# Optimization experiments

Hardware: AMD Instinct MI355X
Metric: run time of the kernel (lower is better)

## Reference

```python
import jax, jax.numpy as jnp
import numpy as np

L, B, D, H = 256, 128, 256, 256


def setup_inputs() -> dict:
    key = jax.random.key(0)
    ks = jax.random.split(key, 24)
    rng = np.random.default_rng(0)
    # random dependency trees: node 0 is root, head[i] < i  => reversed index
    # order (L-1 .. 0) is a valid children-before-parent topological order
    heads = np.zeros((B, L), dtype=np.int64)
    for i in range(1, L):
        heads[:, i] = rng.integers(0, i, size=B)
    parents = np.full((L, B), L, dtype=np.int32)  # parents[node, b]; root -> L (dummy slot)
    parents[1:, :] = heads[:, 1:].T
    indexes = np.tile(np.arange(L - 1, -1, -1, dtype=np.int32)[:, None], (1, B))
    inp = {
        "inputs": jax.random.normal(ks[0], (L, B, D), jnp.float32),
        "indexes": jnp.asarray(indexes),
        "parents": jnp.asarray(parents),
    }
    i = 1
    for pre in ("dt", "td"):
        for nm, out_d, in_d in (("ioux", 3 * H, D), ("iouh", 3 * H, H), ("fx", H, D), ("fh", H, H)):
            s = 1.0 / np.sqrt(in_d)
            inp[f"{pre}_{nm}_w"] = jax.random.uniform(ks[i], (out_d, in_d), jnp.float32, -s, s)
            inp[f"{pre}_{nm}_b"] = jnp.zeros((out_d,), jnp.float32)
            i += 1
    return inp


def _cell(x, sum_c, sum_h, ioux_w, ioux_b, iouh_w, iouh_b, fx_w, fx_b, fh_w, fh_b):
    # tree-LSTM node gating; dropout is identity (eval mode)
    iou = x @ ioux_w.T + ioux_b + sum_h @ iouh_w.T + iouh_b
    i, o, u = jnp.split(iou, 3, axis=1)
    i, o, u = jax.nn.sigmoid(i), jax.nn.sigmoid(o), jnp.tanh(u)
    f = jax.nn.sigmoid(x @ fx_w.T + fx_b + sum_h @ fh_w.T + fh_b)
    c = i * u + f * sum_c
    h = o * jnp.tanh(c)
    return c, h


def _dt(inputs, indexes, parents, params):
    # bottom-up: gather accumulated child sums at node, scatter-add (c,h) to parent
    L_, B_ = indexes.shape
    H_ = params[2].shape[1]
    step_x = jnp.take_along_axis(inputs, indexes[:, :, None], axis=0)  # [L,B,D]
    step_par = jnp.take_along_axis(parents, indexes, axis=0)  # [L,B]
    barange = jnp.arange(B_)

    def step(carry, xs):
        state_c, state_h, acc_c, acc_h = carry
        x, idx, par = xs
        sc = acc_c[barange, idx]  # [B,H] sum of children cells
        sh = acc_h[barange, idx]
        c, h = _cell(x, sc, sh, *params)
        state_c = state_c.at[barange, idx].set(c)
        state_h = state_h.at[barange, idx].set(h)
        acc_c = acc_c.at[barange, par].add(c)  # root's parent -> dummy slot L
        acc_h = acc_h.at[barange, par].add(h)
        return (state_c, state_h, acc_c, acc_h), None

    init = (jnp.zeros((B_, L_, H_), inputs.dtype), jnp.zeros((B_, L_, H_), inputs.dtype),
            jnp.zeros((B_, L_ + 1, H_), inputs.dtype), jnp.zeros((B_, L_ + 1, H_), inputs.dtype))
    (sc, sh, _, _), _ = jax.lax.scan(step, init, (step_x, indexes, step_par))
    return sc.transpose(1, 0, 2), sh.transpose(1, 0, 2)  # [L,B,H]


def _td(inputs, indexes, parents, params):
    # top-down: reversed topological order, gather parent (c,h); root reads zeros (slot L)
    L_, B_ = indexes.shape
    H_ = params[2].shape[1]
    step_x = jnp.take_along_axis(inputs, indexes[:, :, None], axis=0)
    step_par = jnp.take_along_axis(parents, indexes, axis=0)
    barange = jnp.arange(B_)

    def step(carry, xs):
        state_c, state_h = carry  # [B, L+1, H], slot L stays zero
        x, idx, par = xs
        pc = state_c[barange, par]
        ph = state_h[barange, par]
        c, h = _cell(x, pc, ph, *params)
        state_c = state_c.at[barange, idx].set(c)
        state_h = state_h.at[barange, idx].set(h)
        return (state_c, state_h), None

    init = (jnp.zeros((B_, L_ + 1, H_), inputs.dtype), jnp.zeros((B_, L_ + 1, H_), inputs.dtype))
    (sc, sh), _ = jax.lax.scan(step, init, (step_x, indexes, step_par), reverse=True)
    return sc[:, :L_].transpose(1, 0, 2), sh[:, :L_].transpose(1, 0, 2)


def reference(inputs, indexes, parents,
              dt_ioux_w, dt_ioux_b, dt_iouh_w, dt_iouh_b, dt_fx_w, dt_fx_b, dt_fh_w, dt_fh_b,
              td_ioux_w, td_ioux_b, td_iouh_w, td_iouh_b, td_fx_w, td_fx_b, td_fh_w, td_fh_b):
    dt_p = (dt_ioux_w, dt_ioux_b, dt_iouh_w, dt_iouh_b, dt_fx_w, dt_fx_b, dt_fh_w, dt_fh_b)
    td_p = (td_ioux_w, td_ioux_b, td_iouh_w, td_iouh_b, td_fx_w, td_fx_b, td_fh_w, td_fh_b)
    dt_c, dt_h = _dt(inputs, indexes, parents, dt_p)
    td_c, td_h = _td(inputs, indexes, parents, td_p)
    cells = jnp.concatenate((dt_c, td_c), axis=2)  # [L,B,2H]
    hiddens = jnp.concatenate((dt_h, td_h), axis=2)
    return cells, hiddens
```

## Files before the change

kernel.cpp:

```cpp
#include <hip/hip_runtime.h>

#define LL 256
#define BB 128
#define NLEV 48

typedef float  floatx4 __attribute__((ext_vector_type(4)));
typedef short  short8  __attribute__((ext_vector_type(8)));

struct Params {
  const float* inputs;
  const float* ioux_w[2]; const float* ioux_b[2];
  const float* iouh_w[2]; const float* iouh_b[2];
  const float* fx_w[2];   const float* fx_b[2];
  const float* fh_w[2];   const float* fh_b[2];
};

__device__ __forceinline__ unsigned short f2bf(float f) {
  unsigned u = __float_as_uint(f);
  u += 0x7fffu + ((u >> 16) & 1u);
  return (unsigned short)(u >> 16);
}
__device__ __forceinline__ float bf2f(unsigned u) { return __uint_as_float(u << 16); }
__device__ __forceinline__ float sigm(float x) { return 1.0f / (1.0f + __expf(-x)); }
__device__ __forceinline__ float tanh_(float x) { return 1.0f - 2.0f / (1.0f + __expf(2.0f * x)); }

__global__ __launch_bounds__(256) void prep_kernel(Params p,
    unsigned short* a16, unsigned short* w16x, unsigned short* w16h,
    float* bias, int* lvcnt) {
  size_t tid = (size_t)blockIdx.x * blockDim.x + threadIdx.x;
  size_t nth = (size_t)gridDim.x * blockDim.x;

  const float4* in4 = (const float4*)p.inputs;
  for (size_t i = tid; i < 2097152u; i += nth) {
    float4 v = in4[i];
    ((ushort4*)a16)[i] = make_ushort4(f2bf(v.x), f2bf(v.y), f2bf(v.z), f2bf(v.w));
  }
  for (size_t i = tid; i < 524288u; i += nth) {
    int d = (int)(i >> 18); int r = (int)(i & 262143);
    int cc = r >> 8; int k = r & 255;
    float sx = (cc < 768) ? p.ioux_w[d][cc * 256 + k] : p.fx_w[d][(cc - 768) * 256 + k];
    float sh = (cc < 768) ? p.iouh_w[d][cc * 256 + k] : p.fh_w[d][(cc - 768) * 256 + k];
    w16x[i] = f2bf(sx);
    w16h[i] = f2bf(sh);
  }
  for (size_t i = tid; i < 2048u; i += nth) {
    int d = (int)(i >> 10); int cc = (int)(i & 1023);
    bias[i] = (cc < 768) ? (p.ioux_b[d][cc] + p.iouh_b[d][cc])
                         : (p.fx_b[d][cc - 768] + p.fh_b[d][cc - 768]);
  }
  for (size_t i = tid; i < 2u * NLEV; i += nth) lvcnt[i] = 0;
}

__global__ __launch_bounds__(256) void levels_kernel(
    const int* __restrict__ parents, int* __restrict__ lev_g,
    int* __restrict__ csr_off, int* __restrict__ csr_dat, int* __restrict__ lvcnt) {
  __shared__ int parL[256], lvdt[256], lvtd[256];
  __shared__ int cmax[257], ccnt[257], coff[257], ccur[257];
  __shared__ int histd[NLEV], histt[NLEV];
  int b = blockIdx.x, t = threadIdx.x;

  parL[t] = parents[t * BB + b];
  for (int v = t; v < 257; v += 256) { cmax[v] = -1; ccnt[v] = 0; }
  if (t < NLEV) { histd[t] = 0; histt[t] = 0; }
  __syncthreads();

  if (t == 0) {
    lvtd[0] = 0;
    for (int i = 1; i < 256; ++i) lvtd[i] = lvtd[parL[i]] + 1;
  }
  if (t == 1) {
    for (int i = 255; i >= 1; --i) {
      int l = cmax[i] + 1;
      lvdt[i] = l;
      int p = parL[i];
      if (cmax[p] < l) cmax[p] = l;
    }
    lvdt[0] = cmax[0] + 1;
  }
  __syncthreads();

  int l1 = min(lvdt[t], NLEV - 1);
  int l2 = min(lvtd[t], NLEV - 1);
  atomicAdd(&histd[l1], 1);
  atomicAdd(&histt[l2], 1);
  if (t >= 1) atomicAdd(&ccnt[parL[t]], 1);
  lev_g[b * 256 + t] = l1;
  lev_g[32768 + b * 256 + t] = l2;
  __syncthreads();

  if (t == 0) {
    int s = 0;
    for (int i = 0; i < 257; ++i) { coff[i] = s; s += ccnt[i]; }
  }
  __syncthreads();
  for (int v = t; v < 257; v += 256) ccur[v] = coff[v];
  __syncthreads();
  if (t >= 1) {
    int pos = atomicAdd(&ccur[parL[t]], 1);
    csr_dat[b * 256 + pos] = t;
  }
  for (int v = t; v < 257; v += 256) csr_off[b * 260 + v] = coff[v];
  if (t < NLEV) {
    if (histd[t]) atomicAdd(&lvcnt[t], histd[t]);
    if (histt[t]) atomicAdd(&lvcnt[NLEV + t], histt[t]);
  }
}

__global__ __launch_bounds__(128) void scan_kernel(const int* __restrict__ lvcnt,
                                                   int* __restrict__ lvoff,
                                                   int* __restrict__ lvcur) {
  __shared__ int c[2 * NLEV], o[2 * (NLEV + 1)];
  int t = threadIdx.x;
  if (t < 2 * NLEV) c[t] = lvcnt[t];
  __syncthreads();
  if (t < 2) {
    int s = 0;
    for (int l = 0; l < NLEV; ++l) { o[t * (NLEV + 1) + l] = s; s += c[t * NLEV + l]; }
    o[t * (NLEV + 1) + NLEV] = s;
  }
  __syncthreads();
  if (t < 2 * (NLEV + 1)) lvoff[t] = o[t];
  if (t < 2 * NLEV) lvcur[t] = o[(t / NLEV) * (NLEV + 1) + (t % NLEV)];
}

__global__ __launch_bounds__(256) void scatter_kernel(const int* __restrict__ lev_g,
    int* __restrict__ lvcur, unsigned* __restrict__ plist) {
  __shared__ int hist[NLEV], base[NLEV], cnt2[NLEV];
  int b = blockIdx.x, d = blockIdx.y, t = threadIdx.x;
  if (t < NLEV) { hist[t] = 0; cnt2[t] = 0; }
  __syncthreads();
  int l = lev_g[d * 32768 + b * 256 + t];
  atomicAdd(&hist[l], 1);
  __syncthreads();
  if (t < NLEV && hist[t] > 0) base[t] = atomicAdd(&lvcur[d * NLEV + t], hist[t]);
  __syncthreads();
  int r = atomicAdd(&cnt2[l], 1);
  plist[d * 32768 + base[l] + r] = ((unsigned)b << 16) | (unsigned)t;
}

__global__ __launch_bounds__(256) void xproj_gemm(
    const unsigned short* __restrict__ a16,
    const unsigned short* __restrict__ w16x,
    unsigned short* __restrict__ xp) {
  __shared__ unsigned short As[128 * 72], Bs[128 * 72];
  int t = threadIdx.x;
  int w = t >> 6, lane = t & 63, l16 = lane & 15, quad = lane >> 4;
  int m0 = blockIdx.x * 128;
  int d = blockIdx.y >> 3;
  int cc0 = (blockIdx.y & 7) * 128;
  const unsigned short* Bg = w16x + ((size_t)d * 1024 + cc0) * 256;
  int lr = t >> 3, seg = t & 7;

  floatx4 acc[4][4];
#pragma unroll
  for (int i = 0; i < 4; ++i)
#pragma unroll
    for (int j = 0; j < 4; ++j) acc[i][j] = (floatx4){0.f, 0.f, 0.f, 0.f};

  for (int ck = 0; ck < 4; ++ck) {
    int k0 = ck * 64;
#pragma unroll
    for (int it = 0; it < 4; ++it) {
      int row = it * 32 + lr;
      *(uint4*)&As[row * 72 + seg * 8] =
          *(const uint4*)(a16 + (size_t)(m0 + row) * 256 + k0 + seg * 8);
      *(uint4*)&Bs[row * 72 + seg * 8] =
          *(const uint4*)(Bg + (size_t)row * 256 + k0 + seg * 8);
    }
    __syncthreads();
#pragma unroll
    for (int kc = 0; kc < 2; ++kc) {
      int kg = kc * 4 + quad;
      short8 af[4], bf[4];
#pragma unroll
      for (int mf = 0; mf < 4; ++mf)
        af[mf] = *(const short8*)&As[((w & 1) * 64 + mf * 16 + l16) * 72 + kg * 8];
#pragma unroll
      for (int nf = 0; nf < 4; ++nf)
        bf[nf] = *(const short8*)&Bs[((w >> 1) * 64 + nf * 16 + l16) * 72 + kg * 8];
#pragma unroll
      for (int mf = 0; mf < 4; ++mf)
#pragma unroll
        for (int nf = 0; nf < 4; ++nf)
          acc[mf][nf] = __builtin_amdgcn_mfma_f32_16x16x32_bf16(af[mf], bf[nf], acc[mf][nf], 0, 0, 0);
    }
    __syncthreads();
  }
  unsigned short* out = xp + (size_t)d * 33554432u;
#pragma unroll
  for (int mf = 0; mf < 4; ++mf)
#pragma unroll
    for (int nf = 0; nf < 4; ++nf)
#pragma unroll
      for (int r = 0; r < 4; ++r) {
        int row = m0 + (w & 1) * 64 + mf * 16 + quad * 4 + r;
        int col = cc0 + (w >> 1) * 64 + nf * 16 + l16;
        out[(size_t)row * 1024 + col] = f2bf(acc[mf][nf][r]);
      }
}

__global__ __launch_bounds__(256) void gather_kernel(int l,
    const int* __restrict__ lvoff, const unsigned* __restrict__ plist,
    const int* __restrict__ csr_off, const int* __restrict__ csr_dat,
    const int* __restrict__ parents, const float* __restrict__ hidd,
    unsigned short* __restrict__ A16ws) {
  int d = blockIdx.z;
  int i0 = lvoff[d * (NLEV + 1) + l];
  int i1 = lvoff[d * (NLEV + 1) + l + 1];
  int wv = threadIdx.x >> 6, lane = threadIdx.x & 63;
  for (int gi = i0 + blockIdx.x * 4 + wv; gi < i1; gi += 512) {
    unsigned pr = plist[d * 32768 + gi];
    int b = pr >> 16, node = pr & 0xffff;
    float sx = 0.f, sy = 0.f, sz = 0.f, sw = 0.f;
    if (d == 0) {
      int o0 = csr_off[b * 260 + node], o1 = csr_off[b * 260 + node + 1];
      for (int e = o0; e < o1; ++e) {
        int cn = csr_dat[b * 256 + e];
        float4 v = *(const float4*)(hidd + ((size_t)cn * BB + b) * 512 + lane * 4);
        sx += v.x; sy += v.y; sz += v.z; sw += v.w;
      }
    } else {
      int par = parents[node * BB + b];
      if (par != LL) {
        float4 v = *(const float4*)(hidd + ((size_t)par * BB + b) * 512 + 256 + lane * 4);
        sx = v.x; sy = v.y; sz = v.z; sw = v.w;
      }
    }
    *(ushort4*)&A16ws[(size_t)d * 8388608u + (size_t)gi * 256 + lane * 4] =
        make_ushort4(f2bf(sx), f2bf(sy), f2bf(sz), f2bf(sw));
  }
}

__global__ __launch_bounds__(256) void level_gemm(int l,
    const unsigned short* __restrict__ w16h, const float* __restrict__ bias,
    const unsigned short* __restrict__ xp,
    const int* __restrict__ lvoff, const unsigned* __restrict__ plist,
    const int* __restrict__ csr_off, const int* __restrict__ csr_dat,
    const int* __restrict__ parents, const unsigned short* __restrict__ A16ws,
    float* __restrict__ cells, float* __restrict__ hidd) {
  __shared__ unsigned short As[128 * 72], Bs[128 * 72];
  int d = blockIdx.z;
  int i0 = lvoff[d * (NLEV + 1) + l];
  int i1 = lvoff[d * (NLEV + 1) + l + 1];
  int np = i1 - i0;
  if (np <= 0) return;
  int ntiles = (np + 127) >> 7;

  int t = threadIdx.x;
  int w = t >> 6, lane = t & 63, l16 = lane & 15, quad = lane >> 4;
  int j0 = blockIdx.y * 32;
  const unsigned short* Bg = w16h + (size_t)d * 262144u;
  const unsigned short* Ag = A16ws + (size_t)d * 8388608u;
  int lr = t >> 3, seg = t & 7;

  for (int mt = blockIdx.x; mt < ntiles; mt += gridDim.x) {
    floatx4 acc[2][4][2];
#pragma unroll
    for (int mf = 0; mf < 2; ++mf)
#pragma unroll
      for (int g = 0; g < 4; ++g)
#pragma unroll
        for (int js = 0; js < 2; ++js) acc[mf][g][js] = (floatx4){0.f, 0.f, 0.f, 0.f};

    for (int ck = 0; ck < 4; ++ck) {
      int k0 = ck * 64;
#pragma unroll
      for (int it = 0; it < 4; ++it) {
        int row = it * 32 + lr;
        int gi = i0 + mt * 128 + row;
        uint4 av = make_uint4(0u, 0u, 0u, 0u);
        if (gi < i1) av = *(const uint4*)(Ag + (size_t)gi * 256 + k0 + seg * 8);
        *(uint4*)&As[row * 72 + seg * 8] = av;
        int cc = ((row >> 5) << 8) + j0 + (row & 31);
        *(uint4*)&Bs[row * 72 + seg * 8] =
            *(const uint4*)(Bg + (size_t)cc * 256 + k0 + seg * 8);
      }
      __syncthreads();
#pragma unroll
      for (int kc = 0; kc < 2; ++kc) {
        int kg = kc * 4 + quad;
        short8 af[2];
#pragma unroll
        for (int mf = 0; mf < 2; ++mf)
          af[mf] = *(const short8*)&As[(w * 32 + mf * 16 + l16) * 72 + kg * 8];
#pragma unroll
        for (int g = 0; g < 4; ++g)
#pragma unroll
          for (int js = 0; js < 2; ++js) {
            short8 bf = *(const short8*)&Bs[(g * 32 + js * 16 + l16) * 72 + kg * 8];
            acc[0][g][js] = __builtin_amdgcn_mfma_f32_16x16x32_bf16(af[0], bf, acc[0][g][js], 0, 0, 0);
            acc[1][g][js] = __builtin_amdgcn_mfma_f32_16x16x32_bf16(af[1], bf, acc[1][g][js], 0, 0, 0);
          }
      }
      __syncthreads();
    }

#pragma unroll
    for (int mf = 0; mf < 2; ++mf)
#pragma unroll
      for (int r = 0; r < 4; ++r) {
        int row = w * 32 + mf * 16 + quad * 4 + r;
        int gi = i0 + mt * 128 + row;
        if (gi >= i1) continue;
        unsigned pr = plist[d * 32768 + gi];
        int b = pr >> 16, node = pr & 0xffff;
        float sc0 = 0.f, sc1 = 0.f;
        if (d == 0) {
          int o0 = csr_off[b * 260 + node], o1 = csr_off[b * 260 + node + 1];
          for (int e = o0; e < o1; ++e) {
            int cn = csr_dat[b * 256 + e];
            const float* cbase = cells + ((size_t)cn * BB + b) * 512;
            sc0 += cbase[j0 + l16];
            sc1 += cbase[j0 + 16 + l16];
          }
        } else {
          int par = parents[node * BB + b];
          if (par != LL) {
            const float* cbase = cells + ((size_t)par * BB + b) * 512 + 256;
            sc0 = cbase[j0 + l16];
            sc1 = cbase[j0 + 16 + l16];
          }
        }
        const unsigned short* xrow = xp + (size_t)d * 33554432u + ((size_t)node * BB + b) * 1024;
        const float* brow = bias + d * 1024;
#pragma unroll
        for (int js = 0; js < 2; ++js) {
          int j = j0 + js * 16 + l16;
          float sc = js ? sc1 : sc0;
          float pi = acc[mf][0][js][r] + brow[j]       + bf2f(xrow[j]);
          float po = acc[mf][1][js][r] + brow[256 + j] + bf2f(xrow[256 + j]);
          float pu = acc[mf][2][js][r] + brow[512 + j] + bf2f(xrow[512 + j]);
          float pf = acc[mf][3][js][r] + brow[768 + j] + bf2f(xrow[768 + j]);
          float gi_ = sigm(pi), go = sigm(po), gu = tanh_(pu), gf = sigm(pf);
          float c = gi_ * gu + gf * sc;
          float h = go * tanh_(c);
          size_t ob = ((size_t)node * BB + b) * 512 + (d << 8) + j;
          cells[ob] = c;
          hidd[ob] = h;
        }
      }
  }
}

extern "C" void kernel_launch(void* const* d_in, const int* in_sizes, int n_in,
                              void* d_out, int out_size, void* d_ws, size_t ws_size,
                              hipStream_t stream) {
  Params p;
  p.inputs = (const float*)d_in[0];
  const int* parents = (const int*)d_in[2];
  for (int d = 0; d < 2; ++d) {
    int o = 3 + d * 8;
    p.ioux_w[d] = (const float*)d_in[o + 0];
    p.ioux_b[d] = (const float*)d_in[o + 1];
    p.iouh_w[d] = (const float*)d_in[o + 2];
    p.iouh_b[d] = (const float*)d_in[o + 3];
    p.fx_w[d]   = (const float*)d_in[o + 4];
    p.fx_b[d]   = (const float*)d_in[o + 5];
    p.fh_w[d]   = (const float*)d_in[o + 6];
    p.fh_b[d]   = (const float*)d_in[o + 7];
  }

  unsigned short* a16   = (unsigned short*)d_ws;
  unsigned short* w16x  = a16 + 8388608u;
  unsigned short* w16h  = w16x + 524288u;
  unsigned short* xp    = w16h + 524288u;
  unsigned short* A16ws = xp + 67108864u;
  float* bias = (float*)(A16ws + 16777216u);
  int*   lev_g   = (int*)(bias + 2048u);
  int*   csr_off = lev_g + 65536;
  int*   csr_dat = csr_off + 33280;
  int*   lvcnt   = csr_dat + 32768;
  int*   lvoff   = lvcnt + 2 * NLEV;
  int*   lvcur   = lvoff + 2 * (NLEV + 1);
  unsigned* plist = (unsigned*)(lvcur + 2 * NLEV);

  float* cells = (float*)d_out;
  float* hidd  = cells + 16777216u;

  prep_kernel<<<dim3(1024), dim3(256), 0, stream>>>(p, a16, w16x, w16h, bias, lvcnt);
  levels_kernel<<<dim3(128), dim3(256), 0, stream>>>(parents, lev_g, csr_off, csr_dat, lvcnt);
  scan_kernel<<<dim3(1), dim3(128), 0, stream>>>(lvcnt, lvoff, lvcur);
  scatter_kernel<<<dim3(128, 2), dim3(256), 0, stream>>>(lev_g, lvcur, plist);
  xproj_gemm<<<dim3(256, 16), dim3(256), 0, stream>>>(a16, w16x, xp);
  for (int l = 0; l < NLEV; ++l) {
    gather_kernel<<<dim3(128, 1, 2), dim3(256), 0, stream>>>(l, lvoff, plist,
        csr_off, csr_dat, parents, hidd, A16ws);
    level_gemm<<<dim3(32, 8, 2), dim3(256), 0, stream>>>(l, w16h, bias, xp,
        lvoff, plist, csr_off, csr_dat, parents, A16ws, cells, hidd);
  }
}
```

Before: 1.295 ms.

## Fuse per-level gather and GEMM launches into one cooperative persistent kernel

Replaces the 96 per-level kernel launches (a gather and a GEMM for each of 48 levels) with a single cooperative kernel of 256 blocks. The kernel loops over levels and uses grid-wide syncs with device fences between the gather and GEMM phases. The aim is to remove launch overhead and inter-kernel gaps on this latency-bound recursion. In exchange, each level pays two grid barriers, the grid is smaller (16x8x2 instead of 32x8x2), and the code falls back to the old launches if the cooperative launch fails.

```diff
diff --git a/kernel.cpp b/kernel.cpp
--- a/kernel.cpp
+++ b/kernel.cpp
@@ -1,8 +1,13 @@
 #include <hip/hip_runtime.h>
+#include <hip/hip_cooperative_groups.h>
+
+namespace cg = cooperative_groups;
 
 #define LL 256
 #define BB 128
 #define NLEV 48
+
+#define DEV_FENCE() __builtin_amdgcn_fence(__ATOMIC_SEQ_CST, "agent")
 
 typedef float  floatx4 __attribute__((ext_vector_type(4)));
 typedef short  short8  __attribute__((ext_vector_type(8)));
@@ -342,6 +347,156 @@
   }
 }
 
+struct FusedArgs {
+  const unsigned short* w16h; const float* bias; const unsigned short* xp;
+  const int* lvoff; const unsigned* plist;
+  const int* csr_off; const int* csr_dat; const int* parents;
+  unsigned short* A16ws; float* cells; float* hidd;
+};
+
+__global__ __launch_bounds__(256, 2) void levels_fused(FusedArgs a) {
+  __shared__ unsigned short As[128 * 72], Bs[128 * 72];
+  cg::grid_group grid = cg::this_grid();
+
+  int t = threadIdx.x;
+  int w = t >> 6, lane = t & 63, l16 = lane & 15, quad = lane >> 4;
+  int d = blockIdx.z;
+  int gblk = (int)blockIdx.x + (int)blockIdx.y * (int)gridDim.x;
+  int nglb = (int)gridDim.x * (int)gridDim.y;
+  int j0 = blockIdx.y * 32;
+  int lr = t >> 3, seg = t & 7;
+  const unsigned short* Bg = a.w16h + (size_t)d * 262144u;
+  const unsigned short* Ag = a.A16ws + (size_t)d * 8388608u;
+  unsigned short* Aw = a.A16ws + (size_t)d * 8388608u;
+
+  for (int l = 0; l < NLEV; ++l) {
+    int i0d = a.lvoff[l], i1d = a.lvoff[l + 1];
+    int i0t = a.lvoff[(NLEV + 1) + l], i1t = a.lvoff[(NLEV + 1) + l + 1];
+    if (i1d == i0d && i1t == i0t) continue;
+    int i0 = d ? i0t : i0d, i1 = d ? i1t : i1d;
+    int np = i1 - i0;
+
+    for (int gi = i0 + gblk * 4 + w; gi < i1; gi += nglb * 4) {
+      unsigned pr = a.plist[d * 32768 + gi];
+      int b = pr >> 16, node = pr & 0xffff;
+      float sx = 0.f, sy = 0.f, sz = 0.f, sw = 0.f;
+      if (d == 0) {
+        int o0 = a.csr_off[b * 260 + node], o1 = a.csr_off[b * 260 + node + 1];
+        for (int e = o0; e < o1; ++e) {
+          int cn = a.csr_dat[b * 256 + e];
+          float4 v = *(const float4*)(a.hidd + ((size_t)cn * BB + b) * 512 + lane * 4);
+          sx += v.x; sy += v.y; sz += v.z; sw += v.w;
+        }
+      } else {
+        int par = a.parents[node * BB + b];
+        if (par != LL) {
+          float4 v = *(const float4*)(a.hidd + ((size_t)par * BB + b) * 512 + 256 + lane * 4);
+          sx = v.x; sy = v.y; sz = v.z; sw = v.w;
+        }
+      }
+      *(ushort4*)&Aw[(size_t)gi * 256 + lane * 4] =
+          make_ushort4(f2bf(sx), f2bf(sy), f2bf(sz), f2bf(sw));
+    }
+    DEV_FENCE();
+    grid.sync();
+    DEV_FENCE();
+
+    if (np > 0) {
+      int ntiles = (np + 127) >> 7;
+      for (int mt = blockIdx.x; mt < ntiles; mt += gridDim.x) {
+        floatx4 acc[2][4][2];
+#pragma unroll
+        for (int mf = 0; mf < 2; ++mf)
+#pragma unroll
+          for (int g = 0; g < 4; ++g)
+#pragma unroll
+            for (int js = 0; js < 2; ++js) acc[mf][g][js] = (floatx4){0.f, 0.f, 0.f, 0.f};
+
+        for (int ck = 0; ck < 4; ++ck) {
+          int k0 = ck * 64;
+#pragma unroll
+          for (int it = 0; it < 4; ++it) {
+            int row = it * 32 + lr;
+            int gi = i0 + mt * 128 + row;
+            uint4 av = make_uint4(0u, 0u, 0u, 0u);
+            if (gi < i1) av = *(const uint4*)(Ag + (size_t)gi * 256 + k0 + seg * 8);
+            *(uint4*)&As[row * 72 + seg * 8] = av;
+            int cc = ((row >> 5) << 8) + j0 + (row & 31);
+            *(uint4*)&Bs[row * 72 + seg * 8] =
+                *(const uint4*)(Bg + (size_t)cc * 256 + k0 + seg * 8);
+          }
+          __syncthreads();
+#pragma unroll
+          for (int kc = 0; kc < 2; ++kc) {
+            int kg = kc * 4 + quad;
+            short8 af[2];
+#pragma unroll
+            for (int mf = 0; mf < 2; ++mf)
+              af[mf] = *(const short8*)&As[(w * 32 + mf * 16 + l16) * 72 + kg * 8];
+#pragma unroll
+            for (int g = 0; g < 4; ++g)
+#pragma unroll
+              for (int js = 0; js < 2; ++js) {
+                short8 bf = *(const short8*)&Bs[(g * 32 + js * 16 + l16) * 72 + kg * 8];
+                acc[0][g][js] = __builtin_amdgcn_mfma_f32_16x16x32_bf16(af[0], bf, acc[0][g][js], 0, 0, 0);
+                acc[1][g][js] = __builtin_amdgcn_mfma_f32_16x16x32_bf16(af[1], bf, acc[1][g][js], 0, 0, 0);
+              }
+          }
+          __syncthreads();
+        }
+
+#pragma unroll
+        for (int mf = 0; mf < 2; ++mf)
+#pragma unroll
+          for (int r = 0; r < 4; ++r) {
+            int row = w * 32 + mf * 16 + quad * 4 + r;
+            int gi = i0 + mt * 128 + row;
+            if (gi >= i1) continue;
+            unsigned pr = a.plist[d * 32768 + gi];
+            int b = pr >> 16, node = pr & 0xffff;
+            float sc0 = 0.f, sc1 = 0.f;
+            if (d == 0) {
+              int o0 = a.csr_off[b * 260 + node], o1 = a.csr_off[b * 260 + node + 1];
+              for (int e = o0; e < o1; ++e) {
+                int cn = a.csr_dat[b * 256 + e];
+                const float* cbase = a.cells + ((size_t)cn * BB + b) * 512;
+                sc0 += cbase[j0 + l16];
+                sc1 += cbase[j0 + 16 + l16];
+              }
+            } else {
+              int par = a.parents[node * BB + b];
+              if (par != LL) {
+                const float* cbase = a.cells + ((size_t)par * BB + b) * 512 + 256;
+                sc0 = cbase[j0 + l16];
+                sc1 = cbase[j0 + 16 + l16];
+              }
+            }
+            const unsigned short* xrow = a.xp + (size_t)d * 33554432u + ((size_t)node * BB + b) * 1024;
+            const float* brow = a.bias + d * 1024;
+#pragma unroll
+            for (int js = 0; js < 2; ++js) {
+              int j = j0 + js * 16 + l16;
+              float sc = js ? sc1 : sc0;
+              float pi = acc[mf][0][js][r] + brow[j]       + bf2f(xrow[j]);
+              float po = acc[mf][1][js][r] + brow[256 + j] + bf2f(xrow[256 + j]);
+              float pu = acc[mf][2][js][r] + brow[512 + j] + bf2f(xrow[512 + j]);
+              float pf = acc[mf][3][js][r] + brow[768 + j] + bf2f(xrow[768 + j]);
+              float gi_ = sigm(pi), go = sigm(po), gu = tanh_(pu), gf = sigm(pf);
+              float c = gi_ * gu + gf * sc;
+              float h = go * tanh_(c);
+              size_t ob = ((size_t)node * BB + b) * 512 + (d << 8) + j;
+              a.cells[ob] = c;
+              a.hidd[ob] = h;
+            }
+          }
+      }
+    }
+    DEV_FENCE();
+    grid.sync();
+    DEV_FENCE();
+  }
+}
+
 extern "C" void kernel_launch(void* const* d_in, const int* in_sizes, int n_in,
                               void* d_out, int out_size, void* d_ws, size_t ws_size,
                               hipStream_t stream) {
@@ -382,10 +537,21 @@
   scan_kernel<<<dim3(1), dim3(128), 0, stream>>>(lvcnt, lvoff, lvcur);
   scatter_kernel<<<dim3(128, 2), dim3(256), 0, stream>>>(lev_g, lvcur, plist);
   xproj_gemm<<<dim3(256, 16), dim3(256), 0, stream>>>(a16, w16x, xp);
-  for (int l = 0; l < NLEV; ++l) {
-    gather_kernel<<<dim3(128, 1, 2), dim3(256), 0, stream>>>(l, lvoff, plist,
-        csr_off, csr_dat, parents, hidd, A16ws);
-    level_gemm<<<dim3(32, 8, 2), dim3(256), 0, stream>>>(l, w16h, bias, xp,
-        lvoff, plist, csr_off, csr_dat, parents, A16ws, cells, hidd);
-  }
-}
+
+  FusedArgs fa;
+  fa.w16h = w16h; fa.bias = bias; fa.xp = xp;
+  fa.lvoff = lvoff; fa.plist = plist;
+  fa.csr_off = csr_off; fa.csr_dat = csr_dat; fa.parents = parents;
+  fa.A16ws = A16ws; fa.cells = cells; fa.hidd = hidd;
+  void* kargs[] = { &fa };
+  hipError_t cerr = hipLaunchCooperativeKernel((void*)levels_fused, dim3(16, 8, 2),
+                                               dim3(256), kargs, 0, stream);
+  if (cerr != hipSuccess) {
+    for (int l = 0; l < NLEV; ++l) {
+      gather_kernel<<<dim3(128, 1, 2), dim3(256), 0, stream>>>(l, lvoff, plist,
+          csr_off, csr_dat, parents, hidd, A16ws);
+      level_gemm<<<dim3(32, 8, 2), dim3(256), 0, stream>>>(l, w16h, bias, xp,
+          lvoff, plist, csr_off, csr_dat, parents, A16ws, cells, hidd);
+    }
+  }
+}
```

After: 3.130 ms. 2.42x slower.

## Fuse per-level gather and GEMM into one persistent per-batch tree kernel

Applied to the files above, without the earlier changes.

Replaces the 96 per-level gather_kernel/level_gemm launches, plus the scan and scatter kernels, with one persistent kernel launched as one block per (batch, direction). Each block builds its own level ordering in shared memory and walks the levels in sequence. At each level it gathers child or parent hidden sums into a small LDS tile and runs MFMA against the recurrent weights, which prep_kernel now pre-swizzles into fragment order so they can be loaded directly from global memory. The aim is to remove launch overhead and cross-batch synchronisation. The cost is that every small tile re-reads the full weight matrix from L2, and each block relies on seeing its own earlier global writes across levels.

```diff
diff --git a/kernel.cpp b/kernel.cpp
--- a/kernel.cpp
+++ b/kernel.cpp
@@ -41,7 +41,10 @@
     float sx = (cc < 768) ? p.ioux_w[d][cc * 256 + k] : p.fx_w[d][(cc - 768) * 256 + k];
     float sh = (cc < 768) ? p.iouh_w[d][cc * 256 + k] : p.fh_w[d][(cc - 768) * 256 + k];
     w16x[i] = f2bf(sx);
-    w16h[i] = f2bf(sh);
+    int nf = cc >> 4, lcc = cc & 15;
+    int ks = k >> 5, kr = k & 31;
+    int lane = (kr >> 3) * 16 + lcc, e = kr & 7;
+    w16h[((size_t)(d * 64 + nf) * 8 + ks) * 512 + lane * 8 + e] = f2bf(sh);
   }
   for (size_t i = tid; i < 2048u; i += nth) {
     int d = (int)(i >> 10); int cc = (int)(i & 1023);
@@ -56,12 +59,10 @@
     int* __restrict__ csr_off, int* __restrict__ csr_dat, int* __restrict__ lvcnt) {
   __shared__ int parL[256], lvdt[256], lvtd[256];
   __shared__ int cmax[257], ccnt[257], coff[257], ccur[257];
-  __shared__ int histd[NLEV], histt[NLEV];
   int b = blockIdx.x, t = threadIdx.x;
 
   parL[t] = parents[t * BB + b];
   for (int v = t; v < 257; v += 256) { cmax[v] = -1; ccnt[v] = 0; }
-  if (t < NLEV) { histd[t] = 0; histt[t] = 0; }
   __syncthreads();
 
   if (t == 0) {
@@ -81,8 +82,6 @@
 
   int l1 = min(lvdt[t], NLEV - 1);
   int l2 = min(lvtd[t], NLEV - 1);
-  atomicAdd(&histd[l1], 1);
-  atomicAdd(&histt[l2], 1);
   if (t >= 1) atomicAdd(&ccnt[parL[t]], 1);
   lev_g[b * 256 + t] = l1;
   lev_g[32768 + b * 256 + t] = l2;
@@ -100,42 +99,6 @@
     csr_dat[b * 256 + pos] = t;
   }
   for (int v = t; v < 257; v += 256) csr_off[b * 260 + v] = coff[v];
-  if (t < NLEV) {
-    if (histd[t]) atomicAdd(&lvcnt[t], histd[t]);
-    if (histt[t]) atomicAdd(&lvcnt[NLEV + t], histt[t]);
-  }
-}
-
-__global__ __launch_bounds__(128) void scan_kernel(const int* __restrict__ lvcnt,
-                                                   int* __restrict__ lvoff,
-                                                   int* __restrict__ lvcur) {
-  __shared__ int c[2 * NLEV], o[2 * (NLEV + 1)];
-  int t = threadIdx.x;
-  if (t < 2 * NLEV) c[t] = lvcnt[t];
-  __syncthreads();
-  if (t < 2) {
-    int s = 0;
-    for (int l = 0; l < NLEV; ++l) { o[t * (NLEV + 1) + l] = s; s += c[t * NLEV + l]; }
-    o[t * (NLEV + 1) + NLEV] = s;
-  }
-  __syncthreads();
-  if (t < 2 * (NLEV + 1)) lvoff[t] = o[t];
-  if (t < 2 * NLEV) lvcur[t] = o[(t / NLEV) * (NLEV + 1) + (t % NLEV)];
-}
-
-__global__ __launch_bounds__(256) void scatter_kernel(const int* __restrict__ lev_g,
-    int* __restrict__ lvcur, unsigned* __restrict__ plist) {
-  __shared__ int hist[NLEV], base[NLEV], cnt2[NLEV];
-  int b = blockIdx.x, d = blockIdx.y, t = threadIdx.x;
-  if (t < NLEV) { hist[t] = 0; cnt2[t] = 0; }
-  __syncthreads();
-  int l = lev_g[d * 32768 + b * 256 + t];
-  atomicAdd(&hist[l], 1);
-  __syncthreads();
-  if (t < NLEV && hist[t] > 0) base[t] = atomicAdd(&lvcur[d * NLEV + t], hist[t]);
-  __syncthreads();
-  int r = atomicAdd(&cnt2[l], 1);
-  plist[d * 32768 + base[l] + r] = ((unsigned)b << 16) | (unsigned)t;
 }
 
 __global__ __launch_bounds__(256) void xproj_gemm(
@@ -199,146 +162,158 @@
       }
 }
 
-__global__ __launch_bounds__(256) void gather_kernel(int l,
-    const int* __restrict__ lvoff, const unsigned* __restrict__ plist,
-    const int* __restrict__ csr_off, const int* __restrict__ csr_dat,
-    const int* __restrict__ parents, const float* __restrict__ hidd,
-    unsigned short* __restrict__ A16ws) {
-  int d = blockIdx.z;
-  int i0 = lvoff[d * (NLEV + 1) + l];
-  int i1 = lvoff[d * (NLEV + 1) + l + 1];
-  int wv = threadIdx.x >> 6, lane = threadIdx.x & 63;
-  for (int gi = i0 + blockIdx.x * 4 + wv; gi < i1; gi += 512) {
-    unsigned pr = plist[d * 32768 + gi];
-    int b = pr >> 16, node = pr & 0xffff;
-    float sx = 0.f, sy = 0.f, sz = 0.f, sw = 0.f;
-    if (d == 0) {
-      int o0 = csr_off[b * 260 + node], o1 = csr_off[b * 260 + node + 1];
-      for (int e = o0; e < o1; ++e) {
-        int cn = csr_dat[b * 256 + e];
-        float4 v = *(const float4*)(hidd + ((size_t)cn * BB + b) * 512 + lane * 4);
-        sx += v.x; sy += v.y; sz += v.z; sw += v.w;
-      }
-    } else {
-      int par = parents[node * BB + b];
-      if (par != LL) {
-        float4 v = *(const float4*)(hidd + ((size_t)par * BB + b) * 512 + 256 + lane * 4);
-        sx = v.x; sy = v.y; sz = v.z; sw = v.w;
-      }
-    }
-    *(ushort4*)&A16ws[(size_t)d * 8388608u + (size_t)gi * 256 + lane * 4] =
-        make_ushort4(f2bf(sx), f2bf(sy), f2bf(sz), f2bf(sw));
-  }
-}
-
-__global__ __launch_bounds__(256) void level_gemm(int l,
-    const unsigned short* __restrict__ w16h, const float* __restrict__ bias,
+__global__ __launch_bounds__(256, 1) void tree_fused(
+    const int* __restrict__ lev_g, const int* __restrict__ csr_off_g,
+    const int* __restrict__ csr_dat_g, const int* __restrict__ parents,
+    const unsigned short* __restrict__ w16hf, const float* __restrict__ bias,
     const unsigned short* __restrict__ xp,
-    const int* __restrict__ lvoff, const unsigned* __restrict__ plist,
-    const int* __restrict__ csr_off, const int* __restrict__ csr_dat,
-    const int* __restrict__ parents, const unsigned short* __restrict__ A16ws,
     float* __restrict__ cells, float* __restrict__ hidd) {
-  __shared__ unsigned short As[128 * 72], Bs[128 * 72];
-  int d = blockIdx.z;
-  int i0 = lvoff[d * (NLEV + 1) + l];
-  int i1 = lvoff[d * (NLEV + 1) + l + 1];
-  int np = i1 - i0;
-  if (np <= 0) return;
-  int ntiles = (np + 127) >> 7;
-
-  int t = threadIdx.x;
+  __shared__ unsigned short As[32 * 264];
+  __shared__ int lvl[256], ord[256], parL[256], cdat[256];
+  __shared__ int coff[257];
+  __shared__ int hist[NLEV], loff[NLEV + 1], cur[NLEV];
+
+  int b = blockIdx.x, d = blockIdx.y, t = threadIdx.x;
   int w = t >> 6, lane = t & 63, l16 = lane & 15, quad = lane >> 4;
-  int j0 = blockIdx.y * 32;
-  const unsigned short* Bg = w16h + (size_t)d * 262144u;
-  const unsigned short* Ag = A16ws + (size_t)d * 8388608u;
-  int lr = t >> 3, seg = t & 7;
-
-  for (int mt = blockIdx.x; mt < ntiles; mt += gridDim.x) {
-    floatx4 acc[2][4][2];
-#pragma unroll
-    for (int mf = 0; mf < 2; ++mf)
-#pragma unroll
-      for (int g = 0; g < 4; ++g)
-#pragma unroll
-        for (int js = 0; js < 2; ++js) acc[mf][g][js] = (floatx4){0.f, 0.f, 0.f, 0.f};
-
-    for (int ck = 0; ck < 4; ++ck) {
-      int k0 = ck * 64;
-#pragma unroll
-      for (int it = 0; it < 4; ++it) {
-        int row = it * 32 + lr;
-        int gi = i0 + mt * 128 + row;
-        uint4 av = make_uint4(0u, 0u, 0u, 0u);
-        if (gi < i1) av = *(const uint4*)(Ag + (size_t)gi * 256 + k0 + seg * 8);
-        *(uint4*)&As[row * 72 + seg * 8] = av;
-        int cc = ((row >> 5) << 8) + j0 + (row & 31);
-        *(uint4*)&Bs[row * 72 + seg * 8] =
-            *(const uint4*)(Bg + (size_t)cc * 256 + k0 + seg * 8);
+  int gr = t >> 3, gs = t & 7;
+
+  lvl[t]  = lev_g[d * 32768 + b * 256 + t];
+  parL[t] = parents[t * BB + b];
+  cdat[t] = csr_dat_g[b * 256 + t];
+  for (int v = t; v < 257; v += 256) coff[v] = csr_off_g[b * 260 + v];
+  if (t < NLEV) hist[t] = 0;
+  __syncthreads();
+  atomicAdd(&hist[lvl[t]], 1);
+  __syncthreads();
+  if (t == 0) {
+    int s = 0;
+    for (int l = 0; l < NLEV; ++l) { loff[l] = s; s += hist[l]; }
+    loff[NLEV] = s;
+  }
+  __syncthreads();
+  if (t < NLEV) cur[t] = loff[t];
+  __syncthreads();
+  { int pos = atomicAdd(&cur[lvl[t]], 1); ord[pos] = t; }
+  __syncthreads();
+
+  const float* brow = bias + d * 1024;
+  const unsigned short* Wf = w16hf + (size_t)d * 262144u;
+  const unsigned short* xpd = xp + (size_t)d * 33554432u;
+
+  for (int l = 0; l < NLEV; ++l) {
+    int n0 = loff[l], np = loff[l + 1] - n0;
+    if (np == 0) continue;
+    int ntiles = (np + 31) >> 5;
+    for (int mt = 0; mt < ntiles; ++mt) {
+      {
+        int i = mt * 32 + gr;
+        if (i < np) {
+          float a8[32];
+#pragma unroll
+          for (int q = 0; q < 32; ++q) a8[q] = 0.f;
+          int node = ord[n0 + i];
+          if (d == 0) {
+            int o0 = coff[node], o1 = coff[node + 1];
+            for (int e = o0; e < o1; ++e) {
+              const float4* hb = (const float4*)(hidd +
+                  ((size_t)cdat[e] * BB + b) * 512 + gs * 32);
+#pragma unroll
+              for (int q = 0; q < 8; ++q) {
+                float4 v = hb[q];
+                a8[q*4+0] += v.x; a8[q*4+1] += v.y; a8[q*4+2] += v.z; a8[q*4+3] += v.w;
+              }
+            }
+          } else {
+            int par = parL[node];
+            if (par != LL) {
+              const float4* hb = (const float4*)(hidd +
+                  ((size_t)par * BB + b) * 512 + 256 + gs * 32);
+#pragma unroll
+              for (int q = 0; q < 8; ++q) {
+                float4 v = hb[q];
+                a8[q*4+0] = v.x; a8[q*4+1] = v.y; a8[q*4+2] = v.z; a8[q*4+3] = v.w;
+              }
+            }
+          }
+#pragma unroll
+          for (int q = 0; q < 4; ++q) {
+            short8 o;
+#pragma unroll
+            for (int e = 0; e < 8; ++e) o[e] = (short)f2bf(a8[q * 8 + e]);
+            *(short8*)&As[gr * 264 + gs * 32 + q * 8] = o;
+          }
+        }
       }
       __syncthreads();
-#pragma unroll
-      for (int kc = 0; kc < 2; ++kc) {
-        int kg = kc * 4 + quad;
-        short8 af[2];
-#pragma unroll
-        for (int mf = 0; mf < 2; ++mf)
-          af[mf] = *(const short8*)&As[(w * 32 + mf * 16 + l16) * 72 + kg * 8];
+
+      short8 a[2][8];
+#pragma unroll
+      for (int mf = 0; mf < 2; ++mf)
+#pragma unroll
+        for (int ks = 0; ks < 8; ++ks)
+          a[mf][ks] = *(const short8*)&As[(mf * 16 + l16) * 264 + ks * 32 + quad * 8];
+      floatx4 acc[2][4][4];
+#pragma unroll
+      for (int mf = 0; mf < 2; ++mf)
 #pragma unroll
         for (int g = 0; g < 4; ++g)
 #pragma unroll
-          for (int js = 0; js < 2; ++js) {
-            short8 bf = *(const short8*)&Bs[(g * 32 + js * 16 + l16) * 72 + kg * 8];
-            acc[0][g][js] = __builtin_amdgcn_mfma_f32_16x16x32_bf16(af[0], bf, acc[0][g][js], 0, 0, 0);
-            acc[1][g][js] = __builtin_amdgcn_mfma_f32_16x16x32_bf16(af[1], bf, acc[1][g][js], 0, 0, 0);
-          }
-      }
+          for (int jj = 0; jj < 4; ++jj) acc[mf][g][jj] = (floatx4){0.f, 0.f, 0.f, 0.f};
+#pragma unroll
+      for (int ks = 0; ks < 8; ++ks)
+#pragma unroll
+        for (int g = 0; g < 4; ++g)
+#pragma unroll
+          for (int jj = 0; jj < 4; ++jj) {
+            int nf = g * 16 + w * 4 + jj;
+            short8 bf = *(const short8*)(Wf + ((size_t)(nf * 8 + ks) * 64 + lane) * 8);
+            acc[0][g][jj] = __builtin_amdgcn_mfma_f32_16x16x32_bf16(a[0][ks], bf, acc[0][g][jj], 0, 0, 0);
+            acc[1][g][jj] = __builtin_amdgcn_mfma_f32_16x16x32_bf16(a[1][ks], bf, acc[1][g][jj], 0, 0, 0);
+          }
+      __syncthreads();
+
+#pragma unroll
+      for (int mf = 0; mf < 2; ++mf)
+#pragma unroll
+        for (int r = 0; r < 4; ++r) {
+          int i = mt * 32 + mf * 16 + quad * 4 + r;
+          if (i >= np) continue;
+          int node = ord[n0 + i];
+          float scv[4] = {0.f, 0.f, 0.f, 0.f};
+          int jb = w * 64 + l16;
+          if (d == 0) {
+            int o0 = coff[node], o1 = coff[node + 1];
+            for (int e = o0; e < o1; ++e) {
+              const float* cb = cells + ((size_t)cdat[e] * BB + b) * 512;
+              scv[0] += cb[jb];      scv[1] += cb[jb + 16];
+              scv[2] += cb[jb + 32]; scv[3] += cb[jb + 48];
+            }
+          } else {
+            int par = parL[node];
+            if (par != LL) {
+              const float* cb = cells + ((size_t)par * BB + b) * 512 + 256;
+              scv[0] = cb[jb];      scv[1] = cb[jb + 16];
+              scv[2] = cb[jb + 32]; scv[3] = cb[jb + 48];
+            }
+          }
+          const unsigned short* xr = xpd + ((size_t)node * BB + b) * 1024;
+          size_t ob = ((size_t)node * BB + b) * 512 + (d << 8);
+#pragma unroll
+          for (int jj = 0; jj < 4; ++jj) {
+            int j = w * 64 + jj * 16 + l16;
+            float pi = acc[mf][0][jj][r] + brow[j]       + bf2f(xr[j]);
+            float po = acc[mf][1][jj][r] + brow[256 + j] + bf2f(xr[256 + j]);
+            float pu = acc[mf][2][jj][r] + brow[512 + j] + bf2f(xr[512 + j]);
+            float pf = acc[mf][3][jj][r] + brow[768 + j] + bf2f(xr[768 + j]);
+            float gi_ = sigm(pi), go = sigm(po), gu = tanh_(pu), gf = sigm(pf);
+            float c = gi_ * gu + gf * scv[jj];
+            float h = go * tanh_(c);
+            cells[ob + j] = c;
+            hidd[ob + j]  = h;
+          }
+        }
       __syncthreads();
     }
-
-#pragma unroll
-    for (int mf = 0; mf < 2; ++mf)
-#pragma unroll
-      for (int r = 0; r < 4; ++r) {
-        int row = w * 32 + mf * 16 + quad * 4 + r;
-        int gi = i0 + mt * 128 + row;
-        if (gi >= i1) continue;
-        unsigned pr = plist[d * 32768 + gi];
-        int b = pr >> 16, node = pr & 0xffff;
-        float sc0 = 0.f, sc1 = 0.f;
-        if (d == 0) {
-          int o0 = csr_off[b * 260 + node], o1 = csr_off[b * 260 + node + 1];
-          for (int e = o0; e < o1; ++e) {
-            int cn = csr_dat[b * 256 + e];
-            const float* cbase = cells + ((size_t)cn * BB + b) * 512;
-            sc0 += cbase[j0 + l16];
-            sc1 += cbase[j0 + 16 + l16];
-          }
-        } else {
-          int par = parents[node * BB + b];
-          if (par != LL) {
-            const float* cbase = cells + ((size_t)par * BB + b) * 512 + 256;
-            sc0 = cbase[j0 + l16];
-            sc1 = cbase[j0 + 16 + l16];
-          }
-        }
-        const unsigned short* xrow = xp + (size_t)d * 33554432u + ((size_t)node * BB + b) * 1024;
-        const float* brow = bias + d * 1024;
-#pragma unroll
-        for (int js = 0; js < 2; ++js) {
-          int j = j0 + js * 16 + l16;
-          float sc = js ? sc1 : sc0;
-          float pi = acc[mf][0][js][r] + brow[j]       + bf2f(xrow[j]);
-          float po = acc[mf][1][js][r] + brow[256 + j] + bf2f(xrow[256 + j]);
-          float pu = acc[mf][2][js][r] + brow[512 + j] + bf2f(xrow[512 + j]);
-          float pf = acc[mf][3][js][r] + brow[768 + j] + bf2f(xrow[768 + j]);
-          float gi_ = sigm(pi), go = sigm(po), gu = tanh_(pu), gf = sigm(pf);
-          float c = gi_ * gu + gf * sc;
-          float h = go * tanh_(c);
-          size_t ob = ((size_t)node * BB + b) * 512 + (d << 8) + j;
-          cells[ob] = c;
-          hidd[ob] = h;
-        }
-      }
   }
 }
 
@@ -370,22 +345,13 @@
   int*   csr_off = lev_g + 65536;
   int*   csr_dat = csr_off + 33280;
   int*   lvcnt   = csr_dat + 32768;
-  int*   lvoff   = lvcnt + 2 * NLEV;
-  int*   lvcur   = lvoff + 2 * (NLEV + 1);
-  unsigned* plist = (unsigned*)(lvcur + 2 * NLEV);
 
   float* cells = (float*)d_out;
   float* hidd  = cells + 16777216u;
 
   prep_kernel<<<dim3(1024), dim3(256), 0, stream>>>(p, a16, w16x, w16h, bias, lvcnt);
   levels_kernel<<<dim3(128), dim3(256), 0, stream>>>(parents, lev_g, csr_off, csr_dat, lvcnt);
-  scan_kernel<<<dim3(1), dim3(128), 0, stream>>>(lvcnt, lvoff, lvcur);
-  scatter_kernel<<<dim3(128, 2), dim3(256), 0, stream>>>(lev_g, lvcur, plist);
   xproj_gemm<<<dim3(256, 16), dim3(256), 0, stream>>>(a16, w16x, xp);
-  for (int l = 0; l < NLEV; ++l) {
-    gather_kernel<<<dim3(128, 1, 2), dim3(256), 0, stream>>>(l, lvoff, plist,
-        csr_off, csr_dat, parents, hidd, A16ws);
-    level_gemm<<<dim3(32, 8, 2), dim3(256), 0, stream>>>(l, w16h, bias, xp,
-        lvoff, plist, csr_off, csr_dat, parents, A16ws, cells, hidd);
-  }
-}
+  tree_fused<<<dim3(128, 2), dim3(256), 0, stream>>>(lev_g, csr_off, csr_dat,
+      parents, w16h, bias, xp, cells, hidd);
+}
```

After: 1.740 ms. 1.34x slower.
